# Optimization experiments

Measured on AMD Instinct MI355X. Metric: run time of the kernel, lower is better.

Reference implementation:

```python
import jax, jax.numpy as jnp
import numpy as np

N_SRC = 100000
N_DST = 100000
N_EDGES = 1250000
D_FEAT = 64
HIDDEN = 64
OUT = 128


def setup_inputs() -> dict:
    key = jax.random.key(0)
    ks = jax.random.split(key, 9)
    h_src = jax.random.normal(ks[0], (N_SRC, D_FEAT), dtype=jnp.float32)
    h_dst = jax.random.normal(ks[1], (N_DST, D_FEAT), dtype=jnp.float32)
    edge_weight = jax.random.uniform(ks[2], (N_EDGES,), dtype=jnp.float32)
    W1 = jax.random.normal(ks[3], (D_FEAT, HIDDEN), dtype=jnp.float32) / np.sqrt(D_FEAT)
    b1 = jnp.zeros((HIDDEN,), dtype=jnp.float32)
    W2 = jax.random.normal(ks[4], (HIDDEN + D_FEAT, OUT), dtype=jnp.float32) / np.sqrt(HIDDEN + D_FEAT)
    b2 = jnp.zeros((OUT,), dtype=jnp.float32)
    src_idx = jax.random.randint(ks[5], (N_EDGES,), 0, N_SRC, dtype=jnp.int32)
    dst_idx = jax.random.randint(ks[6], (N_EDGES,), 0, N_DST, dtype=jnp.int32)
    return {
        "h_src": h_src, "h_dst": h_dst, "edge_weight": edge_weight,
        "W1": W1, "b1": b1, "W2": W2, "b2": b2,
        "src_idx": src_idx, "dst_idx": dst_idx,
    }


def reference(h_src, h_dst, edge_weight, W1, b1, W2, b2, src_idx, dst_idx):
    # fc_1 with relu on source features: [N_src, H]
    hs = jax.nn.relu(h_src @ W1 + b1)
    # u_mul_e -> sum: edge-weighted scatter-sum into dst nodes
    msg = hs[src_idx] * edge_weight[:, None]                      # [E, H]
    vs = jax.ops.segment_sum(msg, dst_idx, num_segments=N_DST)    # [N_dst, H]
    # copy_e -> sum: per-dst sum of edge weights
    ws = jax.ops.segment_sum(edge_weight, dst_idx, num_segments=N_DST)  # [N_dst]
    ws = jnp.clip(ws, 1.0, None)[:, None]
    nv = vs / ws
    # fc_2 on concat([weighted-mean, h_dst]) with relu
    new = jax.nn.relu(jnp.concatenate([nv, h_dst], axis=-1) @ W2 + b2)
    # global L2 normalization (tf.norm over the full tensor)
    return new / jnp.linalg.norm(new)
```

## Files before the change

### kernel.cpp

```cpp
#include <hip/hip_runtime.h>

#define N_SRC   100000
#define N_DST   100000
#define N_EDGES 1250000
#define D_FEAT  64
#define HIDDEN  64
#define OUT_F   128

#define DPB    128
#define NBUK   782
#define NBLKA  160
#define CHUNK  ((N_EDGES + NBLKA - 1) / NBLKA)
#define NCNT   (NBUK * NBLKA)
#define NB_SC  ((NCNT + 511) / 512)
#define CAPD   2048

__global__ __launch_bounds__(256, 4) void fc1_kernel(
        const float* __restrict__ h_src, const float* __restrict__ W1,
        const float* __restrict__ b1, float* __restrict__ hs) {
    __shared__ float Xs[128][33];
    __shared__ float Ws[32][64];
    const int t  = threadIdx.x;
    const int tr = t >> 3;
    const int tc = t & 7;
    const int base = blockIdx.x * 128;
    float acc[4][8] = {};

    #pragma unroll 1
    for (int kc = 0; kc < 2; ++kc) {
        const int koff = kc * 32;
        #pragma unroll
        for (int i = 0; i < 4; ++i) {
            int fid = i * 256 + t;
            int row = fid >> 3, q = fid & 7;
            int grow = base + row;
            float4 v = make_float4(0.f, 0.f, 0.f, 0.f);
            if (grow < N_SRC)
                v = *(const float4*)&h_src[(size_t)grow * 64 + koff + q * 4];
            Xs[row][q * 4 + 0] = v.x; Xs[row][q * 4 + 1] = v.y;
            Xs[row][q * 4 + 2] = v.z; Xs[row][q * 4 + 3] = v.w;
        }
        #pragma unroll
        for (int i = 0; i < 2; ++i) {
            int fid = i * 256 + t;
            int kk = fid >> 4, q = fid & 15;
            float4 v = *(const float4*)&W1[(size_t)(koff + kk) * HIDDEN + q * 4];
            *(float4*)&Ws[kk][q * 4] = v;
        }
        __syncthreads();
        #pragma unroll 2
        for (int k = 0; k < 32; ++k) {
            float xv[4];
            #pragma unroll
            for (int r = 0; r < 4; ++r) xv[r] = Xs[tr * 4 + r][k];
            const float4 wlo = *(const float4*)&Ws[k][tc * 8];
            const float4 whi = *(const float4*)&Ws[k][tc * 8 + 4];
            #pragma unroll
            for (int r = 0; r < 4; ++r) {
                acc[r][0] = fmaf(xv[r], wlo.x, acc[r][0]);
                acc[r][1] = fmaf(xv[r], wlo.y, acc[r][1]);
                acc[r][2] = fmaf(xv[r], wlo.z, acc[r][2]);
                acc[r][3] = fmaf(xv[r], wlo.w, acc[r][3]);
                acc[r][4] = fmaf(xv[r], whi.x, acc[r][4]);
                acc[r][5] = fmaf(xv[r], whi.y, acc[r][5]);
                acc[r][6] = fmaf(xv[r], whi.z, acc[r][6]);
                acc[r][7] = fmaf(xv[r], whi.w, acc[r][7]);
            }
        }
        __syncthreads();
    }
    #pragma unroll
    for (int r = 0; r < 4; ++r) {
        int grow = base + tr * 4 + r;
        if (grow < N_SRC) {
            #pragma unroll
            for (int j = 0; j < 8; ++j)
                hs[(size_t)grow * 64 + tc * 8 + j] =
                    fmaxf(acc[r][j] + b1[tc * 8 + j], 0.0f);
        }
    }
}

__global__ __launch_bounds__(256) void bucketA_kernel(
        const int* __restrict__ dst, int* __restrict__ bcnt) {
    __shared__ int h[NBUK];
    for (int i = threadIdx.x; i < NBUK; i += 256) h[i] = 0;
    __syncthreads();
    const int lo = blockIdx.x * CHUNK;
    const int hi = min(lo + CHUNK, N_EDGES);
    for (int i = lo + threadIdx.x; i < hi; i += 256)
        atomicAdd(&h[dst[i] >> 7], 1);
    __syncthreads();
    for (int b = threadIdx.x; b < NBUK; b += 256)
        bcnt[b * NBLKA + blockIdx.x] = h[b];
}

__global__ __launch_bounds__(256) void scan_bsum_kernel(
        const int* __restrict__ c, int* __restrict__ bsum, int n) {
    const int t  = threadIdx.x;
    const int i0 = blockIdx.x * 512 + 2 * t;
    int v0 = (i0     < n) ? c[i0]     : 0;
    int v1 = (i0 + 1 < n) ? c[i0 + 1] : 0;
    int s = v0 + v1;
    #pragma unroll
    for (int off = 32; off > 0; off >>= 1) s += __shfl_down(s, off, 64);
    __shared__ int ws[4];
    if ((t & 63) == 0) ws[t >> 6] = s;
    __syncthreads();
    if (t == 0) bsum[blockIdx.x] = ws[0] + ws[1] + ws[2] + ws[3];
}

__global__ __launch_bounds__(256) void scan_boff_kernel(
        const int* __restrict__ bsum, int* __restrict__ boff, int nb) {
    const int t = threadIdx.x, lane = t & 63, w = t >> 6;
    int v = (t < nb) ? bsum[t] : 0;
    int inc = v;
    #pragma unroll
    for (int off = 1; off < 64; off <<= 1) {
        int u = __shfl_up(inc, off, 64);
        if (lane >= off) inc += u;
    }
    __shared__ int wsum[4];
    if (lane == 63) wsum[w] = inc;
    __syncthreads();
    int add = 0;
    for (int i = 0; i < w; ++i) add += wsum[i];
    if (t < nb) boff[t] = add + inc - v;
}

__global__ __launch_bounds__(256) void scan_write_kernel(
        const int* __restrict__ boff, int* __restrict__ c, int n) {
    const int t = threadIdx.x, lane = t & 63, w = t >> 6;
    const int i0 = blockIdx.x * 512 + 2 * t;
    int v0 = (i0     < n) ? c[i0]     : 0;
    int v1 = (i0 + 1 < n) ? c[i0 + 1] : 0;
    int s = v0 + v1;
    int inc = s;
    #pragma unroll
    for (int off = 1; off < 64; off <<= 1) {
        int u = __shfl_up(inc, off, 64);
        if (lane >= off) inc += u;
    }
    __shared__ int wsum[4];
    if (lane == 63) wsum[w] = inc;
    __syncthreads();
    int add = boff[blockIdx.x];
    for (int i = 0; i < w; ++i) add += wsum[i];
    int g = add + inc - s;
    if (i0     < n) c[i0]     = g;
    if (i0 + 1 < n) c[i0 + 1] = g + v0;
}

__global__ __launch_bounds__(256) void bucketC_kernel(
        const int* __restrict__ src, const int* __restrict__ dst,
        const float* __restrict__ ew, const int* __restrict__ bofs,
        int2* __restrict__ bucketed) {
    __shared__ int cur[NBUK];
    for (int b = threadIdx.x; b < NBUK; b += 256)
        cur[b] = bofs[b * NBLKA + blockIdx.x];
    __syncthreads();
    const int lo = blockIdx.x * CHUNK;
    const int hi = min(lo + CHUNK, N_EDGES);
    for (int i = lo + threadIdx.x; i < hi; i += 256) {
        int d = dst[i];
        int b = d >> 7;
        int pos = atomicAdd(&cur[b], 1);
        bucketed[pos] = make_int2(src[i] | ((d & 127) << 17), __float_as_int(ew[i]));
    }
}

__global__ __launch_bounds__(256) void bucketD_kernel(
        const float* __restrict__ hs, const int2* __restrict__ bucketed,
        const int* __restrict__ bofs, float* __restrict__ nv) {
    __shared__ int  cnt[DPB];
    __shared__ int  beg[DPB];
    __shared__ int  ofs[DPB];
    __shared__ int2 sorted[CAPD];
    const int b = blockIdx.x;
    const int t = threadIdx.x;
    const int s = bofs[b * NBLKA];
    const int e = (b + 1 < NBUK) ? bofs[(b + 1) * NBLKA] : N_EDGES;
    const int m = min(e - s, CAPD);

    for (int i = t; i < DPB; i += 256) cnt[i] = 0;
    __syncthreads();
    for (int i = t; i < m; i += 256)
        atomicAdd(&cnt[(bucketed[s + i].x >> 17) & 127], 1);
    __syncthreads();
    if (t < 64) {
        int a0 = cnt[2 * t], a1 = cnt[2 * t + 1];
        int sp = a0 + a1;
        int inc = sp;
        #pragma unroll
        for (int off = 1; off < 64; off <<= 1) {
            int u = __shfl_up(inc, off, 64);
            if (t >= off) inc += u;
        }
        int excl = inc - sp;
        beg[2 * t] = excl;      beg[2 * t + 1] = excl + a0;
        ofs[2 * t] = excl;      ofs[2 * t + 1] = excl + a0;
    }
    __syncthreads();
    for (int i = t; i < m; i += 256) {
        int2 en = bucketed[s + i];
        int p = atomicAdd(&ofs[(en.x >> 17) & 127], 1);
        sorted[p] = en;
    }
    __syncthreads();

    const int lane = t & 63;
    const int wv   = t >> 6;
    for (int j = wv; j < DPB; j += 4) {
        int d = b * DPB + j;
        if (d >= N_DST) continue;
        int lo = beg[j];
        const int hi = ofs[j];
        float acc = 0.0f, wsum = 0.0f;
        for (; lo + 3 < hi; lo += 4) {
            int2 p0 = sorted[lo],     p1 = sorted[lo + 1];
            int2 p2 = sorted[lo + 2], p3 = sorted[lo + 3];
            float w0 = __int_as_float(p0.y), w1 = __int_as_float(p1.y);
            float w2 = __int_as_float(p2.y), w3 = __int_as_float(p3.y);
            float h0 = hs[(size_t)(p0.x & 0x1FFFF) * 64 + lane];
            float h1 = hs[(size_t)(p1.x & 0x1FFFF) * 64 + lane];
            float h2 = hs[(size_t)(p2.x & 0x1FFFF) * 64 + lane];
            float h3 = hs[(size_t)(p3.x & 0x1FFFF) * 64 + lane];
            acc = fmaf(h0, w0, acc);
            acc = fmaf(h1, w1, acc);
            acc = fmaf(h2, w2, acc);
            acc = fmaf(h3, w3, acc);
            wsum += (w0 + w1) + (w2 + w3);
        }
        for (; lo < hi; ++lo) {
            int2 p = sorted[lo];
            float w0 = __int_as_float(p.y);
            acc = fmaf(hs[(size_t)(p.x & 0x1FFFF) * 64 + lane], w0, acc);
            wsum += w0;
        }
        nv[(size_t)d * 64 + lane] = acc / fmaxf(wsum, 1.0f);
    }
}

__global__ __launch_bounds__(256) void fc2_kernel(
        const float* __restrict__ nv, const float* __restrict__ h_dst,
        const float* __restrict__ W2, const float* __restrict__ b2,
        float* __restrict__ out, double* __restrict__ sumsq) {
    __shared__ float Xs[128][33];
    __shared__ float Ws[32][128];
    const int t  = threadIdx.x;
    const int tr = t >> 4;
    const int tc = t & 15;
    const int base = blockIdx.x * 128;
    float acc[8][8] = {};

    #pragma unroll 1
    for (int kc = 0; kc < 4; ++kc) {
        const float* __restrict__ xsrc = (kc < 2) ? nv : h_dst;
        const int koff = (kc & 1) * 32;
        #pragma unroll
        for (int i = 0; i < 4; ++i) {
            int fid = i * 256 + t;
            int row = fid >> 3, q = fid & 7;
            int grow = base + row;
            float4 v = make_float4(0.f, 0.f, 0.f, 0.f);
            if (grow < N_DST)
                v = *(const float4*)&xsrc[(size_t)grow * 64 + koff + q * 4];
            Xs[row][q * 4 + 0] = v.x; Xs[row][q * 4 + 1] = v.y;
            Xs[row][q * 4 + 2] = v.z; Xs[row][q * 4 + 3] = v.w;
        }
        #pragma unroll
        for (int i = 0; i < 4; ++i) {
            int fid = i * 256 + t;
            int kk = fid >> 5, q = fid & 31;
            float4 v = *(const float4*)&W2[(size_t)(kc * 32 + kk) * OUT_F + q * 4];
            *(float4*)&Ws[kk][q * 4] = v;
        }
        __syncthreads();
        #pragma unroll 2
        for (int k = 0; k < 32; ++k) {
            const float4 wa = *(const float4*)&Ws[k][tc * 4];
            const float4 wb = *(const float4*)&Ws[k][64 + tc * 4];
            #pragma unroll
            for (int r = 0; r < 8; ++r) {
                float x = Xs[tr * 8 + r][k];
                acc[r][0] = fmaf(x, wa.x, acc[r][0]);
                acc[r][1] = fmaf(x, wa.y, acc[r][1]);
                acc[r][2] = fmaf(x, wa.z, acc[r][2]);
                acc[r][3] = fmaf(x, wa.w, acc[r][3]);
                acc[r][4] = fmaf(x, wb.x, acc[r][4]);
                acc[r][5] = fmaf(x, wb.y, acc[r][5]);
                acc[r][6] = fmaf(x, wb.z, acc[r][6]);
                acc[r][7] = fmaf(x, wb.w, acc[r][7]);
            }
        }
        __syncthreads();
    }

    double ss = 0.0;
    #pragma unroll
    for (int r = 0; r < 8; ++r) {
        int grow = base + tr * 8 + r;
        if (grow < N_DST) {
            #pragma unroll
            for (int j = 0; j < 4; ++j) {
                float vA = fmaxf(acc[r][j]     + b2[tc * 4 + j],      0.0f);
                float vB = fmaxf(acc[r][j + 4] + b2[64 + tc * 4 + j], 0.0f);
                out[(size_t)grow * OUT_F + tc * 4 + j]      = vA;
                out[(size_t)grow * OUT_F + 64 + tc * 4 + j] = vB;
                ss += (double)vA * vA + (double)vB * vB;
            }
        }
    }
    #pragma unroll
    for (int off = 32; off > 0; off >>= 1) ss += __shfl_down(ss, off, 64);
    if ((t & 63) == 0) atomicAdd(sumsq, ss);
}

__global__ __launch_bounds__(256) void scale_kernel(
        float* __restrict__ out, const double* __restrict__ sumsq, int n4) {
    const float s = (float)(1.0 / sqrt(*sumsq));
    float4* o4 = (float4*)out;
    const int stride = gridDim.x * blockDim.x;
    for (int i = blockIdx.x * blockDim.x + threadIdx.x; i < n4; i += stride) {
        float4 v = o4[i];
        v.x *= s; v.y *= s; v.z *= s; v.w *= s;
        o4[i] = v;
    }
}

extern "C" void kernel_launch(void* const* d_in, const int* in_sizes, int n_in,
                              void* d_out, int out_size, void* d_ws, size_t ws_size,
                              hipStream_t stream) {
    const float* h_src = (const float*)d_in[0];
    const float* h_dst = (const float*)d_in[1];
    const float* ew    = (const float*)d_in[2];
    const float* W1    = (const float*)d_in[3];
    const float* b1    = (const float*)d_in[4];
    const float* W2    = (const float*)d_in[5];
    const float* b2    = (const float*)d_in[6];
    const int*   src   = (const int*)d_in[7];
    const int*   dst   = (const int*)d_in[8];
    float* out = (float*)d_out;

    float*  hs       = out;
    int2*   bucketed = (int2*)((char*)d_out + 25600000);
    int*    bcnt     = (int*)((char*)d_out + 35600000);
    int*    bsum2    = (int*)((char*)d_out + 36104192);
    int*    boff2    = (int*)((char*)d_out + 36105728);
    float*  nv       = (float*)d_ws;
    double* sumsq    = (double*)((char*)d_ws + 25600000);

    hipMemsetAsync(sumsq, 0, 8, stream);

    fc1_kernel<<<(N_SRC + 127) / 128, 256, 0, stream>>>(h_src, W1, b1, hs);
    bucketA_kernel<<<NBLKA, 256, 0, stream>>>(dst, bcnt);
    scan_bsum_kernel<<<NB_SC, 256, 0, stream>>>(bcnt, bsum2, NCNT);
    scan_boff_kernel<<<1, 256, 0, stream>>>(bsum2, boff2, NB_SC);
    scan_write_kernel<<<NB_SC, 256, 0, stream>>>(boff2, bcnt, NCNT);
    bucketC_kernel<<<NBLKA, 256, 0, stream>>>(src, dst, ew, bcnt, bucketed);
    bucketD_kernel<<<NBUK, 256, 0, stream>>>(hs, bucketed, bcnt, nv);
    fc2_kernel<<<(N_DST + 127) / 128, 256, 0, stream>>>(nv, h_dst, W2, b2, out, sumsq);
    scale_kernel<<<2048, 256, 0, stream>>>(out, sumsq, N_DST * OUT_F / 4);
}
```

Measured before the change: 228.0 us.

## Split fc1 tiles across bucket kernels and transpose fc2 X tile

The fc1 GEMM is split into two halves whose tiles run as extra blocks inside the bucket-count and bucket-scatter kernels, so the dense work overlaps the latency-bound histogram and scatter passes and one launch is removed. Shared memory is a union so both roles fit in one kernel. Separately, fc2 stores its X tile transposed so each thread reads its 8 rows with two float4 LDS loads instead of 8 scalar loads. The fused kernels now carry fc1's register and shared-memory footprint, which may limit occupancy for the bucket blocks.

```diff
diff --git a/kernel.cpp b/kernel.cpp
--- a/kernel.cpp
+++ b/kernel.cpp
@@ -14,16 +14,22 @@
 #define NCNT   (NBUK * NBLKA)
 #define NB_SC  ((NCNT + 511) / 512)
 #define CAPD   2048
-
-__global__ __launch_bounds__(256, 4) void fc1_kernel(
+#define NT_FC1 782
+#define NT_A   391
+#define NT_C   (NT_FC1 - NT_A)
+
+struct FC1SM {
+    float Xs[128][33];
+    float Ws[32][64];
+};
+
+__device__ __forceinline__ void fc1_tile(FC1SM& sm, int tile,
         const float* __restrict__ h_src, const float* __restrict__ W1,
         const float* __restrict__ b1, float* __restrict__ hs) {
-    __shared__ float Xs[128][33];
-    __shared__ float Ws[32][64];
     const int t  = threadIdx.x;
     const int tr = t >> 3;
     const int tc = t & 7;
-    const int base = blockIdx.x * 128;
+    const int base = tile * 128;
     float acc[4][8] = {};
 
     #pragma unroll 1
@@ -37,24 +43,24 @@
             float4 v = make_float4(0.f, 0.f, 0.f, 0.f);
             if (grow < N_SRC)
                 v = *(const float4*)&h_src[(size_t)grow * 64 + koff + q * 4];
-            Xs[row][q * 4 + 0] = v.x; Xs[row][q * 4 + 1] = v.y;
-            Xs[row][q * 4 + 2] = v.z; Xs[row][q * 4 + 3] = v.w;
+            sm.Xs[row][q * 4 + 0] = v.x; sm.Xs[row][q * 4 + 1] = v.y;
+            sm.Xs[row][q * 4 + 2] = v.z; sm.Xs[row][q * 4 + 3] = v.w;
         }
         #pragma unroll
         for (int i = 0; i < 2; ++i) {
             int fid = i * 256 + t;
             int kk = fid >> 4, q = fid & 15;
             float4 v = *(const float4*)&W1[(size_t)(koff + kk) * HIDDEN + q * 4];
-            *(float4*)&Ws[kk][q * 4] = v;
+            *(float4*)&sm.Ws[kk][q * 4] = v;
         }
         __syncthreads();
         #pragma unroll 2
         for (int k = 0; k < 32; ++k) {
             float xv[4];
             #pragma unroll
-            for (int r = 0; r < 4; ++r) xv[r] = Xs[tr * 4 + r][k];
-            const float4 wlo = *(const float4*)&Ws[k][tc * 8];
-            const float4 whi = *(const float4*)&Ws[k][tc * 8 + 4];
+            for (int r = 0; r < 4; ++r) xv[r] = sm.Xs[tr * 4 + r][k];
+            const float4 wlo = *(const float4*)&sm.Ws[k][tc * 8];
+            const float4 whi = *(const float4*)&sm.Ws[k][tc * 8 + 4];
             #pragma unroll
             for (int r = 0; r < 4; ++r) {
                 acc[r][0] = fmaf(xv[r], wlo.x, acc[r][0]);
@@ -81,18 +87,24 @@
     }
 }
 
-__global__ __launch_bounds__(256) void bucketA_kernel(
-        const int* __restrict__ dst, int* __restrict__ bcnt) {
-    __shared__ int h[NBUK];
-    for (int i = threadIdx.x; i < NBUK; i += 256) h[i] = 0;
+__global__ __launch_bounds__(256, 4) void fusedA_kernel(
+        const int* __restrict__ dst, int* __restrict__ bcnt,
+        const float* __restrict__ h_src, const float* __restrict__ W1,
+        const float* __restrict__ b1, float* __restrict__ hs) {
+    __shared__ union { int h[NBUK]; FC1SM g; } sm;
+    if (blockIdx.x >= NBLKA) {
+        fc1_tile(sm.g, blockIdx.x - NBLKA, h_src, W1, b1, hs);
+        return;
+    }
+    for (int i = threadIdx.x; i < NBUK; i += 256) sm.h[i] = 0;
     __syncthreads();
     const int lo = blockIdx.x * CHUNK;
     const int hi = min(lo + CHUNK, N_EDGES);
     for (int i = lo + threadIdx.x; i < hi; i += 256)
-        atomicAdd(&h[dst[i] >> 7], 1);
+        atomicAdd(&sm.h[dst[i] >> 7], 1);
     __syncthreads();
     for (int b = threadIdx.x; b < NBUK; b += 256)
-        bcnt[b * NBLKA + blockIdx.x] = h[b];
+        bcnt[b * NBLKA + blockIdx.x] = sm.h[b];
 }
 
 __global__ __launch_bounds__(256) void scan_bsum_kernel(
@@ -151,20 +163,26 @@
     if (i0 + 1 < n) c[i0 + 1] = g + v0;
 }
 
-__global__ __launch_bounds__(256) void bucketC_kernel(
+__global__ __launch_bounds__(256, 4) void fusedC_kernel(
         const int* __restrict__ src, const int* __restrict__ dst,
         const float* __restrict__ ew, const int* __restrict__ bofs,
-        int2* __restrict__ bucketed) {
-    __shared__ int cur[NBUK];
+        int2* __restrict__ bucketed,
+        const float* __restrict__ h_src, const float* __restrict__ W1,
+        const float* __restrict__ b1, float* __restrict__ hs) {
+    __shared__ union { int cur[NBUK]; FC1SM g; } sm;
+    if (blockIdx.x >= NBLKA) {
+        fc1_tile(sm.g, blockIdx.x - NBLKA + NT_A, h_src, W1, b1, hs);
+        return;
+    }
     for (int b = threadIdx.x; b < NBUK; b += 256)
-        cur[b] = bofs[b * NBLKA + blockIdx.x];
+        sm.cur[b] = bofs[b * NBLKA + blockIdx.x];
     __syncthreads();
     const int lo = blockIdx.x * CHUNK;
     const int hi = min(lo + CHUNK, N_EDGES);
     for (int i = lo + threadIdx.x; i < hi; i += 256) {
         int d = dst[i];
         int b = d >> 7;
-        int pos = atomicAdd(&cur[b], 1);
+        int pos = atomicAdd(&sm.cur[b], 1);
         bucketed[pos] = make_int2(src[i] | ((d & 127) << 17), __float_as_int(ew[i]));
     }
 }
@@ -245,7 +263,7 @@
         const float* __restrict__ nv, const float* __restrict__ h_dst,
         const float* __restrict__ W2, const float* __restrict__ b2,
         float* __restrict__ out, double* __restrict__ sumsq) {
-    __shared__ float Xs[128][33];
+    __shared__ float Xt[32][132];
     __shared__ float Ws[32][128];
     const int t  = threadIdx.x;
     const int tr = t >> 4;
@@ -265,8 +283,10 @@
             float4 v = make_float4(0.f, 0.f, 0.f, 0.f);
             if (grow < N_DST)
                 v = *(const float4*)&xsrc[(size_t)grow * 64 + koff + q * 4];
-            Xs[row][q * 4 + 0] = v.x; Xs[row][q * 4 + 1] = v.y;
-            Xs[row][q * 4 + 2] = v.z; Xs[row][q * 4 + 3] = v.w;
+            Xt[q * 4 + 0][row] = v.x;
+            Xt[q * 4 + 1][row] = v.y;
+            Xt[q * 4 + 2][row] = v.z;
+            Xt[q * 4 + 3][row] = v.w;
         }
         #pragma unroll
         for (int i = 0; i < 4; ++i) {
@@ -278,19 +298,21 @@
         __syncthreads();
         #pragma unroll 2
         for (int k = 0; k < 32; ++k) {
+            const float4 xa = *(const float4*)&Xt[k][tr * 8];
+            const float4 xb = *(const float4*)&Xt[k][tr * 8 + 4];
             const float4 wa = *(const float4*)&Ws[k][tc * 4];
             const float4 wb = *(const float4*)&Ws[k][64 + tc * 4];
+            float xr[8] = {xa.x, xa.y, xa.z, xa.w, xb.x, xb.y, xb.z, xb.w};
             #pragma unroll
             for (int r = 0; r < 8; ++r) {
-                float x = Xs[tr * 8 + r][k];
-                acc[r][0] = fmaf(x, wa.x, acc[r][0]);
-                acc[r][1] = fmaf(x, wa.y, acc[r][1]);
-                acc[r][2] = fmaf(x, wa.z, acc[r][2]);
-                acc[r][3] = fmaf(x, wa.w, acc[r][3]);
-                acc[r][4] = fmaf(x, wb.x, acc[r][4]);
-                acc[r][5] = fmaf(x, wb.y, acc[r][5]);
-                acc[r][6] = fmaf(x, wb.z, acc[r][6]);
-                acc[r][7] = fmaf(x, wb.w, acc[r][7]);
+                acc[r][0] = fmaf(xr[r], wa.x, acc[r][0]);
+                acc[r][1] = fmaf(xr[r], wa.y, acc[r][1]);
+                acc[r][2] = fmaf(xr[r], wa.z, acc[r][2]);
+                acc[r][3] = fmaf(xr[r], wa.w, acc[r][3]);
+                acc[r][4] = fmaf(xr[r], wb.x, acc[r][4]);
+                acc[r][5] = fmaf(xr[r], wb.y, acc[r][5]);
+                acc[r][6] = fmaf(xr[r], wb.z, acc[r][6]);
+                acc[r][7] = fmaf(xr[r], wb.w, acc[r][7]);
             }
         }
         __syncthreads();
@@ -352,12 +374,12 @@
 
     hipMemsetAsync(sumsq, 0, 8, stream);
 
-    fc1_kernel<<<(N_SRC + 127) / 128, 256, 0, stream>>>(h_src, W1, b1, hs);
-    bucketA_kernel<<<NBLKA, 256, 0, stream>>>(dst, bcnt);
+    fusedA_kernel<<<NBLKA + NT_A, 256, 0, stream>>>(dst, bcnt, h_src, W1, b1, hs);
     scan_bsum_kernel<<<NB_SC, 256, 0, stream>>>(bcnt, bsum2, NCNT);
     scan_boff_kernel<<<1, 256, 0, stream>>>(bsum2, boff2, NB_SC);
     scan_write_kernel<<<NB_SC, 256, 0, stream>>>(boff2, bcnt, NCNT);
-    bucketC_kernel<<<NBLKA, 256, 0, stream>>>(src, dst, ew, bcnt, bucketed);
+    fusedC_kernel<<<NBLKA + NT_C, 256, 0, stream>>>(src, dst, ew, bcnt, bucketed,
+                                                    h_src, W1, b1, hs);
     bucketD_kernel<<<NBUK, 256, 0, stream>>>(hs, bucketed, bcnt, nv);
     fc2_kernel<<<(N_DST + 127) / 128, 256, 0, stream>>>(nv, h_dst, W2, b2, out, sumsq);
     scale_kernel<<<2048, 256, 0, stream>>>(out, sumsq, N_DST * OUT_F / 4);
```

Measured after the change: 214.2 us. 1.06x faster.
